# Kernel tuning notes

Measured on AMD Instinct MI355X. Metric: run time of the kernel, lower is better.

Reference implementation:

```python
import jax, jax.numpy as jnp
from jax import lax
import numpy as np

EPS = 1e-5  # BatchNorm eps (inference mode; dropouts are identity in eval)


def _proj(img, w, g, b, m, v, stride):
    """All-heads Conv2d(3x3, no bias) + BatchNorm (inference) fused across heads.
    img: [B, Cin, H, W]; w: [heads, Cout, Cin, 3, 3]; g/b/m/v: [heads, Cout].
    Returns [B, heads, Cout, N'] (channels-first token layout)."""
    heads, Cout, Cin = w.shape[0], w.shape[1], w.shape[2]
    y = lax.conv_general_dilated(
        img, w.reshape(heads * Cout, Cin, 3, 3),
        window_strides=(stride, stride), padding=[(1, 1), (1, 1)],
        dimension_numbers=('NCHW', 'OIHW', 'NCHW'))
    B = y.shape[0]
    N = y.shape[2] * y.shape[3]
    y = y.reshape(B, heads, Cout, N)
    scale = g / jnp.sqrt(v + EPS)               # [heads, Cout]
    shift = b - m * scale
    return y * scale[None, :, :, None] + shift[None, :, :, None]


def reference(x, y, w_conv, bn_gamma, bn_beta, bn_mean, bn_var, w_out1, w_out2, h, w):
    B, N, C = x.shape
    xi = x.reshape(B, h, w, C).transpose(0, 3, 1, 2)  # b (h w) c -> b c h w
    yi = y.reshape(B, h, w, C).transpose(0, 3, 1, 2)
    scale_attn = C ** -0.5

    def P(i, img, stride):
        return _proj(img, w_conv[i], bn_gamma[i], bn_beta[i], bn_mean[i], bn_var[i], stride)

    # torch: query1(x), query2(y), key1(y), key2(x), value1(y), value2(x)
    Q1 = P(0, xi, 2)  # [B,h,C,Nq]
    Q2 = P(1, yi, 2)
    K1 = P(2, yi, 2)
    K2 = P(3, xi, 2)
    V1 = P(4, yi, 1)  # [B,h,C,Nv]
    V2 = P(5, xi, 1)

    # channel-attention: scores are [B, heads, C, C], softmax over last axis
    s1 = jnp.einsum('bhcn,bhdn->bhcd', Q2, K1) * scale_attn
    s2 = jnp.einsum('bhcn,bhdn->bhcd', Q1, K2) * scale_attn
    p1 = jax.nn.softmax(s1, axis=-1)
    p2 = jax.nn.softmax(s2, axis=-1)

    # context [B,heads,C,Nv] -> mean over heads -> [B,Nv,C]
    c1 = jnp.einsum('bhcd,bhdn->bhcn', p1, V1).mean(axis=1).transpose(0, 2, 1)
    c2 = jnp.einsum('bhcd,bhdn->bhcn', p2, V2).mean(axis=1).transpose(0, 2, 1)

    o1 = c1 @ w_out1.T  # Linear(dim_in, dim_out, bias=False)
    o2 = c2 @ w_out2.T
    return o1, o2


def setup_inputs() -> dict:
    B, C, HEADS, H, W = 8, 256, 4, 64, 64
    key = jax.random.key(0)
    ks = jax.random.split(key, 9)
    conv_std = 1.0 / np.sqrt(C * 9)
    lin_std = 1.0 / np.sqrt(C)
    return {
        'x': jax.random.normal(ks[0], (B, H * W, C), jnp.float32),
        'y': jax.random.normal(ks[1], (B, H * W, C), jnp.float32),
        'w_conv': jax.random.normal(ks[2], (6, HEADS, C, C, 3, 3), jnp.float32) * conv_std,
        'bn_gamma': jax.random.uniform(ks[3], (6, HEADS, C), jnp.float32, 0.5, 1.5),
        'bn_beta': jax.random.normal(ks[4], (6, HEADS, C), jnp.float32) * 0.1,
        'bn_mean': jax.random.normal(ks[5], (6, HEADS, C), jnp.float32) * 0.1,
        'bn_var': jax.random.uniform(ks[6], (6, HEADS, C), jnp.float32, 0.5, 1.5),
        'w_out1': jax.random.normal(ks[7], (C, C), jnp.float32) * lin_std,
        'w_out2': jax.random.normal(ks[8], (C, C), jnp.float32) * lin_std,
        'h': H,
        'w': W,
    }
```

## Files before the change

kernel.cpp:

```cpp
#include <hip/hip_runtime.h>
#include <stdint.h>

typedef __bf16 bf16_t;
typedef __bf16 bf16x8 __attribute__((ext_vector_type(8)));
typedef float f32x4 __attribute__((ext_vector_type(4)));

#define EPSBN 1e-5f

#define OFF_XP   ((size_t)0)
#define SZ_IMG   ((size_t)8*4356*256*2)
#define OFF_YP   (OFF_XP + SZ_IMG)
#define OFF_WQS  (OFF_YP + SZ_IMG)
#define SZ_WQS   ((size_t)4*1024*2304*2)
#define OFF_WVT  (OFF_WQS + SZ_WQS)
#define SZ_WVT   ((size_t)2*2304*1024*2)
#define OFF_W1B  (OFF_WVT + SZ_WVT)
#define SZ_WO    ((size_t)65536*2)
#define OFF_W2B  (OFF_W1B + SZ_WO)
#define OFF_SHQ  (OFF_W2B + SZ_WO)
#define SZ_SHQ   ((size_t)4096*4)
#define OFF_SHV  (OFF_SHQ + SZ_SHQ)
#define SZ_SHV   ((size_t)2048*4)
#define OFF_QK   (OFF_SHV + SZ_SHV)
#define SZ_QK    ((size_t)4*8*1024*1024*2)
#define OFF_S    (OFF_QK + SZ_QK)
#define SZ_S     ((size_t)2*8*4*65536*4)
#define OFF_PT   (OFF_S + SZ_S)
#define SZ_PT    ((size_t)2*8*4*65536*2)
#define OFF_A1   (OFF_PT + SZ_PT)
#define SZ_A1    ((size_t)2*8*256*1024*2)
#define OFF_WEFF (OFF_A1 + SZ_A1)
#define SZ_WEFF  ((size_t)2*8*256*2304*2)
#define OFF_BIAS (OFF_WEFF + SZ_WEFF)
#define SZ_BIAS  ((size_t)2*8*256*4)
#define WS_NEED  (OFF_BIAS + SZ_BIAS)

__device__ __forceinline__ void gload16(const bf16_t* g, bf16_t* l) {
  __builtin_amdgcn_global_load_lds(
      (const __attribute__((address_space(1))) void*)g,
      (__attribute__((address_space(3))) void*)l,
      16, 0, 0);
}

__device__ __forceinline__ int lb_off0() { return ((threadIdx.x >> 6)    ) * 512; }
__device__ __forceinline__ int lb_off1() { return ((threadIdx.x >> 6) + 4) * 512; }

#define SBAR0 __builtin_amdgcn_sched_barrier(0)

template<int BSRC>
__device__ __forceinline__ void gemm_core(
    const bf16_t* __restrict__ A, int ldA,
    const bf16_t* __restrict__ B, int ldB,
    int m0, int n0, int KT, f32x4 acc[4][4])
{
  __shared__ bf16_t lA[2][4096];
  __shared__ bf16_t lB[2][4096];
  const int tid  = threadIdx.x;
  const int lane = tid & 63;
  const int wv   = tid >> 6;
  const int wr   = wv >> 1, wc = wv & 1;
  const int r4   = lane >> 2;
  const int k8   = (lane & 3) * 8;

  const bf16_t* gA0 = A + (size_t)(m0 + (wv    )*16 + r4) * ldA + k8;
  const bf16_t* gA1 = A + (size_t)(m0 + (wv + 4)*16 + r4) * ldA + k8;
  const int la0 = (wv    ) * 512;
  const int la1 = (wv + 4) * 512;
  const bf16_t* gB0 = B + (size_t)(n0 + (wv    )*16 + r4) * ldB + k8;
  const bf16_t* gB1 = B + (size_t)(n0 + (wv + 4)*16 + r4) * ldB + k8;
  (void)BSRC;

#pragma unroll
  for (int i = 0; i < 4; ++i)
#pragma unroll
    for (int j = 0; j < 4; ++j)
      acc[i][j] = f32x4{0.f, 0.f, 0.f, 0.f};

  const int lr = lane & 15;
  const int lk = (lane >> 4) * 8;
  int aidx[4], bidx[4];
#pragma unroll
  for (int f = 0; f < 4; ++f) {
    aidx[f] = (wr*64 + f*16 + lr)*32 + lk;
    bidx[f] = (wc*64 + f*16 + lr)*32 + lk;
  }

  auto stage = [&](int bufp, int kt) {
    const int kb = kt * 32;
    gload16(gA0 + kb, &lA[bufp][la0]);
    gload16(gA1 + kb, &lA[bufp][la1]);
    gload16(gB0 + kb, &lB[bufp][lb_off0()]);
    gload16(gB1 + kb, &lB[bufp][lb_off1()]);
  };

  stage(0, 0);
  __syncthreads();
  int buf = 0;
  for (int kt = 0; kt < KT; ++kt) {
    if (kt + 1 < KT) stage(buf ^ 1, kt + 1);
    bf16x8 av[4], bvv[4];
#pragma unroll
    for (int f = 0; f < 4; ++f) av[f]  = *(const bf16x8*)&lA[buf][aidx[f]];
#pragma unroll
    for (int f = 0; f < 4; ++f) bvv[f] = *(const bf16x8*)&lB[buf][bidx[f]];
#pragma unroll
    for (int i = 0; i < 4; ++i)
#pragma unroll
      for (int j = 0; j < 4; ++j)
        acc[i][j] = __builtin_amdgcn_mfma_f32_16x16x32_bf16(av[i], bvv[j], acc[i][j], 0, 0, 0);
    __syncthreads();
    buf ^= 1;
  }
}

template<int STRIDE>
__device__ __forceinline__ void conv256_core(
    const bf16_t* __restrict__ A, const bf16_t* __restrict__ img,
    int m0, int n0, f32x4 acc[8][4])
{
  __shared__ bf16_t lds[4][2][8192];
  const int tid  = threadIdx.x;
  const int lane = tid & 63;
  const int w    = tid >> 6;
  const int wm   = w >> 2;
  const int wn   = w & 3;

#pragma unroll
  for (int f = 0; f < 8; ++f)
#pragma unroll
    for (int j = 0; j < 4; ++j)
      acc[f][j] = f32x4{0.f, 0.f, 0.f, 0.f};

  const int srow = tid >> 2;
  const int ksX  = (tid & 3) ^ ((tid >> 3) & 3);
  const bf16_t* gA0 = A + (size_t)(m0 + srow) * 2304 + ksX*8;
  const bf16_t* gA1 = gA0 + (size_t)128 * 2304;
  const int tk0 = n0 + srow, tk1 = tk0 + 128;
  int px0, px1;
  if (STRIDE == 1) { px0 = (tk0>>6)*66 + (tk0&63);       px1 = (tk1>>6)*66 + (tk1&63); }
  else             { px0 = ((tk0>>5)*2)*66 + (tk0&31)*2; px1 = ((tk1>>5)*2)*66 + (tk1&31)*2; }
  const bf16_t* gB0 = img + (size_t)px0*256 + ksX*8;
  const bf16_t* gB1 = img + (size_t)px1*256 + ksX*8;

  auto stageHalf = [&](int half) {
    const int s = half & 3;
    bf16_t* dA = &lds[s][0][0] + tid*8;
    gload16(gA0 + half*32, dA);
    gload16(gA1 + half*32, dA + 4096);
    const int T = half >> 1, kh = half & 1;
    const int tap = T >> 2;
    const int ky  = (tap >= 6) ? 2 : ((tap >= 3) ? 1 : 0);
    const int kx  = tap - ky*3;
    const int ps  = (ky*66 + kx)*256 + (T & 3)*64 + kh*32;
    bf16_t* dB = &lds[s][1][0] + tid*8;
    gload16(gB0 + ps, dB);
    gload16(gB1 + ps, dB + 4096);
  };

  const int lr    = lane & 15;
  const int slotS = (lane >> 4) ^ ((lane & 6) >> 1);
  int offA[8], offB[4];
#pragma unroll
  for (int f = 0; f < 8; ++f)  offA[f] = (wm*128 + f*16 + lr)*32 + slotS*8;
#pragma unroll
  for (int n = 0; n < 4; ++n)  offB[n] = (wn*64  + n*16 + lr)*32 + slotS*8;

#define LOADREGS(HALF, AV, BV) do {                                        \
    const int s_ = (HALF) & 3;                                             \
    const bf16_t* pA_ = &lds[s_][0][0];                                    \
    const bf16_t* pB_ = &lds[s_][1][0];                                    \
    _Pragma("unroll") for (int f_ = 0; f_ < 8; ++f_)                       \
      AV[f_] = *(const bf16x8*)(pA_ + offA[f_]);                           \
    _Pragma("unroll") for (int n_ = 0; n_ < 4; ++n_)                       \
      BV[n_] = *(const bf16x8*)(pB_ + offB[n_]);                           \
  } while (0)

#define MFMA32(AV, BV) do {                                                \
    __builtin_amdgcn_s_setprio(1);                                         \
    _Pragma("unroll") for (int f_ = 0; f_ < 8; ++f_)                       \
      _Pragma("unroll") for (int n_ = 0; n_ < 4; ++n_)                     \
        acc[f_][n_] = __builtin_amdgcn_mfma_f32_16x16x32_bf16(             \
            AV[f_], BV[n_], acc[f_][n_], 0, 0, 0);                         \
    __builtin_amdgcn_s_setprio(0);                                         \
  } while (0)

  stageHalf(0); stageHalf(1); stageHalf(2);
  SBAR0;
  asm volatile("s_waitcnt vmcnt(4)" ::: "memory");
  SBAR0;
  __builtin_amdgcn_s_barrier();
  SBAR0;

  bf16x8 avP[8], bvP[4], avN[8], bvN[4];
  LOADREGS(0, avP, bvP);

  for (int h = 0; h < 72; h += 2) {
    if (h + 3 < 72) stageHalf(h + 3);
    LOADREGS(h + 1, avN, bvN);
    SBAR0;
    if (h < 69) { asm volatile("s_waitcnt vmcnt(4)" ::: "memory"); }
    else        { asm volatile("s_waitcnt vmcnt(0)" ::: "memory"); }
    SBAR0;
    asm volatile("s_waitcnt lgkmcnt(12)" ::: "memory");
    SBAR0;
    MFMA32(avP, bvP);
    __builtin_amdgcn_s_barrier();
    SBAR0;

    const int h1 = h + 1;
    if (h1 + 3 < 72) stageHalf(h1 + 3);
    if (h1 < 71) {
      LOADREGS(h1 + 1, avP, bvP);
      SBAR0;
      if (h1 < 69) { asm volatile("s_waitcnt vmcnt(4)" ::: "memory"); }
      else         { asm volatile("s_waitcnt vmcnt(0)" ::: "memory"); }
      SBAR0;
      asm volatile("s_waitcnt lgkmcnt(12)" ::: "memory");
      SBAR0;
    } else {
      SBAR0;
      asm volatile("s_waitcnt lgkmcnt(0)" ::: "memory");
      SBAR0;
    }
    MFMA32(avN, bvN);
    __builtin_amdgcn_s_barrier();
    SBAR0;
  }
#undef LOADREGS
#undef MFMA32
}

__global__ __launch_bounds__(512, 2) void k_conv_qk2(const bf16_t* __restrict__ wqs,
    const bf16_t* __restrict__ xp, const bf16_t* __restrict__ yp,
    bf16_t* __restrict__ qk, const float* __restrict__ shq)
{
  const int bx = blockIdx.x, b = blockIdx.y, ci = blockIdx.z;
  const int mt = bx >> 2, nt = bx & 3;
  const int m0 = mt*256, n0 = nt*256;
  const bf16_t* A = wqs + (size_t)ci * 1024 * 2304;
  const bf16_t* img = (((ci == 0) | (ci == 3)) ? xp : yp) + (size_t)b*4356*256;
  f32x4 acc[8][4];
  conv256_core<2>(A, img, m0, n0, acc);

  bf16_t* out = qk + (size_t)(ci*8 + b) * 1024 * 1024;
  const float* sh = shq + ci*1024;
  const int lane = threadIdx.x & 63, w = threadIdx.x >> 6;
  const int wm = w >> 2, wn = w & 3;
#pragma unroll
  for (int f = 0; f < 8; ++f) {
    const int row0 = m0 + wm*128 + f*16 + ((lane >> 4) << 2);
    const f32x4 s4 = *(const f32x4*)&sh[row0];
#pragma unroll
    for (int nf = 0; nf < 4; ++nf) {
      const int col = n0 + wn*64 + nf*16 + (lane & 15);
#pragma unroll
      for (int r = 0; r < 4; ++r)
        out[(size_t)(row0 + r)*1024 + col] = (bf16_t)(acc[f][nf][r] + s4[r]);
    }
  }
}

__global__ __launch_bounds__(512, 2) void k_conv_out2(const bf16_t* __restrict__ weff,
    const bf16_t* __restrict__ xp, const bf16_t* __restrict__ yp,
    const float* __restrict__ bias, float* __restrict__ dout)
{
  const int nt = blockIdx.x, b = blockIdx.y, br = blockIdx.z;
  const int n0 = nt*256;
  const bf16_t* A = weff + (size_t)(br*8 + b)*589824;
  const bf16_t* img = ((br == 0) ? yp : xp) + (size_t)b*4356*256;
  f32x4 acc[8][4];
  conv256_core<1>(A, img, 0, n0, acc);

  float* outp = dout + (size_t)br*8388608 + (size_t)b*1048576;
  const float* bp = bias + (size_t)(br*8 + b)*256;
  const int lane = threadIdx.x & 63, w = threadIdx.x >> 6;
  const int wm = w >> 2, wn = w & 3;
#pragma unroll
  for (int f = 0; f < 8; ++f) {
    const int e0 = wm*128 + f*16 + ((lane >> 4) << 2);
    const f32x4 bv4 = *(const f32x4*)&bp[e0];
#pragma unroll
    for (int nf = 0; nf < 4; ++nf) {
      const int tok = n0 + wn*64 + nf*16 + (lane & 15);
      f32x4 v = acc[f][nf] + bv4;
      *(f32x4*)&outp[(size_t)tok*256 + e0] = v;
    }
  }
}

__global__ __launch_bounds__(256) void k_pack(const float* __restrict__ x, const float* __restrict__ y,
                                              bf16_t* __restrict__ xp, bf16_t* __restrict__ yp)
{
  const int p  = blockIdx.x;
  const int b  = blockIdx.y;
  const int im = blockIdx.z;
  const int c  = threadIdx.x;
  const int i = p / 66, j = p - i*66;
  const float* src = im ? y : x;
  bf16_t* dst = im ? yp : xp;
  float v = 0.f;
  if (i >= 1 && i <= 64 && j >= 1 && j <= 64)
    v = src[((size_t)b*4096 + (size_t)(i-1)*64 + (j-1))*256 + c];
  dst[((size_t)b*4356 + p)*256 + c] = (bf16_t)v;
}

__global__ __launch_bounds__(256) void k_prep_wq(const float* __restrict__ wcv,
    const float* __restrict__ g, const float* __restrict__ be,
    const float* __restrict__ mu, const float* __restrict__ va,
    bf16_t* __restrict__ wqs, float* __restrict__ shq)
{
  const int blk = blockIdx.x;
  __shared__ float lw[2304];
  const float* src = wcv + (size_t)blk * 2304;
  for (int t = threadIdx.x; t < 2304; t += 256) lw[t] = src[t];
  const float sc = g[blk] * rsqrtf(va[blk] + EPSBN);
  if (threadIdx.x == 0) shq[blk] = be[blk] - mu[blk]*sc;
  __syncthreads();
  bf16_t* dst = wqs + (size_t)blk * 2304;
  for (int t = threadIdx.x; t < 2304; t += 256) {
    const int tap = t >> 8, c = t & 255;
    dst[t] = (bf16_t)(lw[c*9 + tap] * sc);
  }
}

__global__ __launch_bounds__(256) void k_prep_wv(const float* __restrict__ wcv,
    const float* __restrict__ g, const float* __restrict__ va,
    bf16_t* __restrict__ wvT)
{
  const int cch = blockIdx.x;
  const int h = blockIdx.y >> 2, dc = blockIdx.y & 3;
  const int br = blockIdx.z;
  __shared__ float lw[64][72];
  __shared__ float lsc[64];
  const int ci = 4 + br;
  const int c0 = cch*8, d0 = dc*64;
  for (int e = threadIdx.x; e < 64*72; e += 256) {
    const int dd = e / 72, q = e - dd*72;
    lw[dd][q] = wcv[(size_t)(ci*1024 + h*256 + d0 + dd)*2304 + c0*9 + q];
  }
  if (threadIdx.x < 64) {
    const int bnIdx = ci*1024 + h*256 + d0 + threadIdx.x;
    lsc[threadIdx.x] = g[bnIdx] * rsqrtf(va[bnIdx] + EPSBN);
  }
  __syncthreads();
  for (int e = threadIdx.x; e < 72*64; e += 256) {
    const int kq = e >> 6, dd = e & 63;
    const int cc = kq / 9, tap = kq - cc*9;
    const int kp = tap*256 + c0 + cc;
    wvT[(size_t)br*2359296 + (size_t)kp*1024 + h*256 + d0 + dd] =
        (bf16_t)(lw[dd][cc*9 + tap] * lsc[dd]);
  }
}

__global__ __launch_bounds__(256) void k_small(const float* __restrict__ w1, const float* __restrict__ w2,
    const float* __restrict__ g, const float* __restrict__ be,
    const float* __restrict__ mu, const float* __restrict__ va,
    bf16_t* __restrict__ w1b, bf16_t* __restrict__ w2b, float* __restrict__ shv)
{
  const int idx = blockIdx.x*256 + threadIdx.x;
  if (idx < 65536) {
    w1b[idx] = (bf16_t)w1[idx];
  } else if (idx < 131072) {
    w2b[idx - 65536] = (bf16_t)w2[idx - 65536];
  } else if (idx < 133120) {
    const int t = idx - 131072;
    const int bnIdx = 4096 + t;
    const float sc = g[bnIdx] * rsqrtf(va[bnIdx] + EPSBN);
    shv[t] = be[bnIdx] - mu[bnIdx]*sc;
  }
}

__global__ __launch_bounds__(256) void k_gemm_s(const bf16_t* __restrict__ qk, float* __restrict__ sb)
{
  const int bx = blockIdx.x, by = blockIdx.y, br = blockIdx.z;
  const int mt = bx >> 1, nt = bx & 1;
  const int b = by >> 2, h = by & 3;
  const int ai = (br == 0) ? 1 : 0;
  const int bi = (br == 0) ? 2 : 3;
  const bf16_t* A  = qk + ((size_t)(ai*8 + b)*1024 + h*256) * 1024;
  const bf16_t* Bp = qk + ((size_t)(bi*8 + b)*1024 + h*256) * 1024;
  f32x4 acc[4][4];
  gemm_core<0>(A, 1024, Bp, 1024, mt*128, nt*128, 32, acc);

  float* out = sb + ((size_t)(br*8 + b)*4 + h) * 65536;
  const int lane = threadIdx.x & 63, wv = threadIdx.x >> 6;
  const int wr = wv >> 1, wc = wv & 1;
#pragma unroll
  for (int i = 0; i < 4; ++i) {
    const int row0 = mt*128 + wr*64 + i*16 + ((lane >> 4) << 2);
#pragma unroll
    for (int j = 0; j < 4; ++j) {
      const int col = nt*128 + wc*64 + j*16 + (lane & 15);
#pragma unroll
      for (int r = 0; r < 4; ++r)
        out[(size_t)(row0 + r)*256 + col] = acc[i][j][r];
    }
  }
}

__global__ __launch_bounds__(256) void k_softmax(const float* __restrict__ sb, bf16_t* __restrict__ pt)
{
  const int cc = blockIdx.x;
  const int bh = blockIdx.y;
  const int br = blockIdx.z;
  const size_t base = ((size_t)br*32 + bh) * 65536;
  __shared__ bf16_t lp[32][256];
  const int tid = threadIdx.x, lane = tid & 63, wv = tid >> 6;
  for (int r = 0; r < 8; ++r) {
    const int row = wv*8 + r;
    const float* srow = sb + base + (size_t)(cc*32 + row)*256;
    f32x4 v = ((const f32x4*)srow)[lane];
    v *= 0.0625f;
    float m = fmaxf(fmaxf(v[0], v[1]), fmaxf(v[2], v[3]));
#pragma unroll
    for (int o = 32; o; o >>= 1) m = fmaxf(m, __shfl_xor(m, o));
    const float e0 = __expf(v[0]-m), e1 = __expf(v[1]-m), e2 = __expf(v[2]-m), e3 = __expf(v[3]-m);
    float s = e0+e1+e2+e3;
#pragma unroll
    for (int o = 32; o; o >>= 1) s += __shfl_xor(s, o);
    const float inv = 0.25f / s;
    lp[row][lane*4+0] = (bf16_t)(e0*inv);
    lp[row][lane*4+1] = (bf16_t)(e1*inv);
    lp[row][lane*4+2] = (bf16_t)(e2*inv);
    lp[row][lane*4+3] = (bf16_t)(e3*inv);
  }
  __syncthreads();
  bf16_t* dst = pt + base;
  for (int it = 0; it < 32; ++it) {
    const int idx = it*256 + tid;
    const int d = idx >> 5, c = idx & 31;
    dst[(size_t)d*256 + cc*32 + c] = lp[c][d];
  }
}

__global__ __launch_bounds__(256) void k_gemm_a(const bf16_t* __restrict__ w1b, const bf16_t* __restrict__ w2b,
    const bf16_t* __restrict__ pt, bf16_t* __restrict__ a1)
{
  const int bx = blockIdx.x, by = blockIdx.y, br = blockIdx.z;
  const int mt = bx >> 1, nt = bx & 1;
  const int b = by >> 2, h = by & 3;
  const bf16_t* A  = br ? w2b : w1b;
  const bf16_t* Bp = pt + ((size_t)(br*8 + b)*4 + h) * 65536;
  f32x4 acc[4][4];
  gemm_core<0>(A, 256, Bp, 256, mt*128, nt*128, 8, acc);

  bf16_t* out = a1 + (size_t)(br*8 + b)*262144 + h*256;
  const int lane = threadIdx.x & 63, wv = threadIdx.x >> 6;
  const int wr = wv >> 1, wc = wv & 1;
#pragma unroll
  for (int i = 0; i < 4; ++i) {
    const int row0 = mt*128 + wr*64 + i*16 + ((lane >> 4) << 2);
#pragma unroll
    for (int j = 0; j < 4; ++j) {
      const int col = nt*128 + wc*64 + j*16 + (lane & 15);
#pragma unroll
      for (int r = 0; r < 4; ++r)
        out[(size_t)(row0 + r)*1024 + col] = (bf16_t)acc[i][j][r];
    }
  }
}

__global__ __launch_bounds__(256) void k_bias(const bf16_t* __restrict__ a1,
    const float* __restrict__ shv, float* __restrict__ bias)
{
  const int wv = threadIdx.x >> 6, lane = threadIdx.x & 63;
  const int e = blockIdx.x*4 + wv;
  const int b = blockIdx.y, br = blockIdx.z;
  const bf16_t* row = a1 + ((size_t)(br*8 + b)*256 + e)*1024;
  const float* sv = shv + br*1024;
  float acc = 0.f;
#pragma unroll
  for (int t = 0; t < 16; ++t) {
    const int idx = t*64 + lane;
    acc += (float)row[idx] * sv[idx];
  }
#pragma unroll
  for (int o = 32; o; o >>= 1) acc += __shfl_xor(acc, o);
  if (lane == 0) bias[(size_t)(br*8 + b)*256 + e] = acc;
}

__global__ __launch_bounds__(256) void k_gemm_weff(const bf16_t* __restrict__ a1,
    const bf16_t* __restrict__ wvT, bf16_t* __restrict__ weff)
{
  const int bx = blockIdx.x, b = blockIdx.y, br = blockIdx.z;
  const int mt = bx / 18, nt = bx - mt*18;
  const bf16_t* A  = a1 + (size_t)(br*8 + b)*262144;
  const bf16_t* Bp = wvT + (size_t)br*2359296;
  f32x4 acc[4][4];
  gemm_core<0>(A, 1024, Bp, 1024, mt*128, nt*128, 32, acc);

  bf16_t* out = weff + (size_t)(br*8 + b)*589824;
  const int lane = threadIdx.x & 63, wv = threadIdx.x >> 6;
  const int wr = wv >> 1, wc = wv & 1;
#pragma unroll
  for (int i = 0; i < 4; ++i) {
    const int row0 = mt*128 + wr*64 + i*16 + ((lane >> 4) << 2);
#pragma unroll
    for (int j = 0; j < 4; ++j) {
      const int col = nt*128 + wc*64 + j*16 + (lane & 15);
#pragma unroll
      for (int r = 0; r < 4; ++r)
        out[(size_t)(row0 + r)*2304 + col] = (bf16_t)acc[i][j][r];
    }
  }
}

extern "C" void kernel_launch(void* const* d_in, const int* in_sizes, int n_in,
                              void* d_out, int out_size, void* d_ws, size_t ws_size,
                              hipStream_t stream)
{
  (void)in_sizes; (void)n_in; (void)out_size;
  const float* x   = (const float*)d_in[0];
  const float* y   = (const float*)d_in[1];
  const float* wcv = (const float*)d_in[2];
  const float* bg  = (const float*)d_in[3];
  const float* bb  = (const float*)d_in[4];
  const float* bm  = (const float*)d_in[5];
  const float* bvv = (const float*)d_in[6];
  const float* w1  = (const float*)d_in[7];
  const float* w2  = (const float*)d_in[8];
  float* out = (float*)d_out;
  char* ws = (char*)d_ws;
  if (ws_size < WS_NEED) return;

  bf16_t* xp   = (bf16_t*)(ws + OFF_XP);
  bf16_t* yp   = (bf16_t*)(ws + OFF_YP);
  bf16_t* wqs  = (bf16_t*)(ws + OFF_WQS);
  bf16_t* wvT  = (bf16_t*)(ws + OFF_WVT);
  bf16_t* w1b  = (bf16_t*)(ws + OFF_W1B);
  bf16_t* w2b  = (bf16_t*)(ws + OFF_W2B);
  float*  shq  = (float*)(ws + OFF_SHQ);
  float*  shv  = (float*)(ws + OFF_SHV);
  bf16_t* qk   = (bf16_t*)(ws + OFF_QK);
  float*  sb   = (float*)(ws + OFF_S);
  bf16_t* pt   = (bf16_t*)(ws + OFF_PT);
  bf16_t* a1   = (bf16_t*)(ws + OFF_A1);
  bf16_t* weff = (bf16_t*)(ws + OFF_WEFF);
  float*  bias = (float*)(ws + OFF_BIAS);

  k_pack     <<<dim3(4356, 8, 2), 256, 0, stream>>>(x, y, xp, yp);
  k_prep_wq  <<<dim3(4096), 256, 0, stream>>>(wcv, bg, bb, bm, bvv, wqs, shq);
  k_prep_wv  <<<dim3(32, 16, 2), 256, 0, stream>>>(wcv, bg, bvv, wvT);
  k_small    <<<dim3(520), 256, 0, stream>>>(w1, w2, bg, bb, bm, bvv, w1b, w2b, shv);
  k_conv_qk2 <<<dim3(16, 8, 4), 512, 0, stream>>>(wqs, xp, yp, qk, shq);
  k_gemm_s   <<<dim3(4, 32, 2), 256, 0, stream>>>(qk, sb);
  k_softmax  <<<dim3(8, 32, 2), 256, 0, stream>>>(sb, pt);
  k_gemm_a   <<<dim3(4, 32, 2), 256, 0, stream>>>(w1b, w2b, pt, a1);
  k_bias     <<<dim3(64, 8, 2), 256, 0, stream>>>(a1, shv, bias);
  k_gemm_weff<<<dim3(36, 8, 2), 256, 0, stream>>>(a1, wvT, weff);
  k_conv_out2<<<dim3(16, 8, 2), 512, 0, stream>>>(weff, xp, yp, bias, out);
}
```

Before: 368.4 us.

## Shrink conv tiles to 256x128 with six-stage LDS pipeline and batch-fastest grid

The shared implicit-GEMM conv core now computes 256x128 output tiles instead of 256x256. Each wave handles 64x64 instead of 128x64, and the B operand is staged as a single 128-token slab. The LDS ring deepens from 4 to 6 stages, so global loads are issued five steps ahead, and the register double-buffer is replaced by a per-step load then MFMA with barriers. Both conv launches move to a 1D grid with batch as the fastest index, doubling block counts to better fill the CUs and group blocks that share weights. In exchange, each block reuses its operands less and pays more barriers per step.

```diff
diff --git a/kernel.cpp b/kernel.cpp
--- a/kernel.cpp
+++ b/kernel.cpp
@@ -114,37 +114,37 @@
 }
 
 template<int STRIDE>
-__device__ __forceinline__ void conv256_core(
+__device__ __forceinline__ void conv128_core(
     const bf16_t* __restrict__ A, const bf16_t* __restrict__ img,
-    int m0, int n0, f32x4 acc[8][4])
-{
-  __shared__ bf16_t lds[4][2][8192];
+    int m0, int n0, f32x4 acc[4][4])
+{
+  __shared__ bf16_t ldsA[6][8192];
+  __shared__ bf16_t ldsB[6][4096];
   const int tid  = threadIdx.x;
   const int lane = tid & 63;
   const int w    = tid >> 6;
-  const int wm   = w >> 2;
-  const int wn   = w & 3;
-
-#pragma unroll
-  for (int f = 0; f < 8; ++f)
-#pragma unroll
-    for (int j = 0; j < 4; ++j)
-      acc[f][j] = f32x4{0.f, 0.f, 0.f, 0.f};
+  const int wm   = w >> 1;
+  const int wn   = w & 1;
+
+#pragma unroll
+  for (int f = 0; f < 4; ++f)
+#pragma unroll
+    for (int c = 0; c < 4; ++c)
+      acc[f][c] = f32x4{0.f, 0.f, 0.f, 0.f};
 
   const int srow = tid >> 2;
   const int ksX  = (tid & 3) ^ ((tid >> 3) & 3);
   const bf16_t* gA0 = A + (size_t)(m0 + srow) * 2304 + ksX*8;
   const bf16_t* gA1 = gA0 + (size_t)128 * 2304;
-  const int tk0 = n0 + srow, tk1 = tk0 + 128;
-  int px0, px1;
-  if (STRIDE == 1) { px0 = (tk0>>6)*66 + (tk0&63);       px1 = (tk1>>6)*66 + (tk1&63); }
-  else             { px0 = ((tk0>>5)*2)*66 + (tk0&31)*2; px1 = ((tk1>>5)*2)*66 + (tk1&31)*2; }
+  const int tk0 = n0 + srow;
+  int px0;
+  if (STRIDE == 1) px0 = (tk0>>6)*66 + (tk0&63);
+  else             px0 = ((tk0>>5)*2)*66 + (tk0&31)*2;
   const bf16_t* gB0 = img + (size_t)px0*256 + ksX*8;
-  const bf16_t* gB1 = img + (size_t)px1*256 + ksX*8;
 
   auto stageHalf = [&](int half) {
-    const int s = half & 3;
-    bf16_t* dA = &lds[s][0][0] + tid*8;
+    const int sl = half % 6;
+    bf16_t* dA = &ldsA[sl][0] + tid*8;
     gload16(gA0 + half*32, dA);
     gload16(gA1 + half*32, dA + 4096);
     const int T = half >> 1, kh = half & 1;
@@ -152,137 +152,120 @@
     const int ky  = (tap >= 6) ? 2 : ((tap >= 3) ? 1 : 0);
     const int kx  = tap - ky*3;
     const int ps  = (ky*66 + kx)*256 + (T & 3)*64 + kh*32;
-    bf16_t* dB = &lds[s][1][0] + tid*8;
-    gload16(gB0 + ps, dB);
-    gload16(gB1 + ps, dB + 4096);
+    gload16(gB0 + ps, &ldsB[sl][0] + tid*8);
   };
 
   const int lr    = lane & 15;
   const int slotS = (lane >> 4) ^ ((lane & 6) >> 1);
-  int offA[8], offB[4];
-#pragma unroll
-  for (int f = 0; f < 8; ++f)  offA[f] = (wm*128 + f*16 + lr)*32 + slotS*8;
-#pragma unroll
-  for (int n = 0; n < 4; ++n)  offB[n] = (wn*64  + n*16 + lr)*32 + slotS*8;
-
-#define LOADREGS(HALF, AV, BV) do {                                        \
-    const int s_ = (HALF) & 3;                                             \
-    const bf16_t* pA_ = &lds[s_][0][0];                                    \
-    const bf16_t* pB_ = &lds[s_][1][0];                                    \
-    _Pragma("unroll") for (int f_ = 0; f_ < 8; ++f_)                       \
-      AV[f_] = *(const bf16x8*)(pA_ + offA[f_]);                           \
-    _Pragma("unroll") for (int n_ = 0; n_ < 4; ++n_)                       \
-      BV[n_] = *(const bf16x8*)(pB_ + offB[n_]);                           \
-  } while (0)
-
-#define MFMA32(AV, BV) do {                                                \
-    __builtin_amdgcn_s_setprio(1);                                         \
-    _Pragma("unroll") for (int f_ = 0; f_ < 8; ++f_)                       \
-      _Pragma("unroll") for (int n_ = 0; n_ < 4; ++n_)                     \
-        acc[f_][n_] = __builtin_amdgcn_mfma_f32_16x16x32_bf16(             \
-            AV[f_], BV[n_], acc[f_][n_], 0, 0, 0);                         \
-    __builtin_amdgcn_s_setprio(0);                                         \
-  } while (0)
-
-  stageHalf(0); stageHalf(1); stageHalf(2);
+  int offA[4], offB[4];
+#pragma unroll
+  for (int f = 0; f < 4; ++f) offA[f] = (wm*64 + f*16 + lr)*32 + slotS*8;
+#pragma unroll
+  for (int c = 0; c < 4; ++c) offB[c] = (wn*64 + c*16 + lr)*32 + slotS*8;
+
+  stageHalf(0); stageHalf(1); stageHalf(2); stageHalf(3); stageHalf(4);
   SBAR0;
-  asm volatile("s_waitcnt vmcnt(4)" ::: "memory");
+  asm volatile("s_waitcnt vmcnt(12)" ::: "memory");
   SBAR0;
   __builtin_amdgcn_s_barrier();
   SBAR0;
 
-  bf16x8 avP[8], bvP[4], avN[8], bvN[4];
-  LOADREGS(0, avP, bvP);
-
-  for (int h = 0; h < 72; h += 2) {
-    if (h + 3 < 72) stageHalf(h + 3);
-    LOADREGS(h + 1, avN, bvN);
+  for (int p = 0; p < 72; ++p) {
+    const int sl = p % 6;
+    const bf16_t* pA = &ldsA[sl][0];
+    const bf16_t* pB = &ldsB[sl][0];
+    bf16x8 av[4], bv[4];
+#pragma unroll
+    for (int f = 0; f < 4; ++f) av[f] = *(const bf16x8*)(pA + offA[f]);
+#pragma unroll
+    for (int c = 0; c < 4; ++c) bv[c] = *(const bf16x8*)(pB + offB[c]);
+    if (p + 5 < 72) stageHalf(p + 5);
     SBAR0;
-    if (h < 69) { asm volatile("s_waitcnt vmcnt(4)" ::: "memory"); }
-    else        { asm volatile("s_waitcnt vmcnt(0)" ::: "memory"); }
+    if      (p < 67)  { asm volatile("s_waitcnt vmcnt(12)" ::: "memory"); }
+    else if (p == 67) { asm volatile("s_waitcnt vmcnt(9)"  ::: "memory"); }
+    else if (p == 68) { asm volatile("s_waitcnt vmcnt(6)"  ::: "memory"); }
+    else if (p == 69) { asm volatile("s_waitcnt vmcnt(3)"  ::: "memory"); }
+    else if (p == 70) { asm volatile("s_waitcnt vmcnt(0)"  ::: "memory"); }
     SBAR0;
-    asm volatile("s_waitcnt lgkmcnt(12)" ::: "memory");
+    asm volatile("s_waitcnt lgkmcnt(4)" ::: "memory");
     SBAR0;
-    MFMA32(avP, bvP);
+    __builtin_amdgcn_s_barrier();
+    asm volatile("s_waitcnt lgkmcnt(0)" ::: "memory");
+    SBAR0;
+    __builtin_amdgcn_s_setprio(1);
+#pragma unroll
+    for (int f = 0; f < 4; ++f)
+#pragma unroll
+      for (int c = 0; c < 4; ++c)
+        acc[f][c] = __builtin_amdgcn_mfma_f32_16x16x32_bf16(av[f], bv[c], acc[f][c], 0, 0, 0);
+    __builtin_amdgcn_s_setprio(0);
     __builtin_amdgcn_s_barrier();
     SBAR0;
-
-    const int h1 = h + 1;
-    if (h1 + 3 < 72) stageHalf(h1 + 3);
-    if (h1 < 71) {
-      LOADREGS(h1 + 1, avP, bvP);
-      SBAR0;
-      if (h1 < 69) { asm volatile("s_waitcnt vmcnt(4)" ::: "memory"); }
-      else         { asm volatile("s_waitcnt vmcnt(0)" ::: "memory"); }
-      SBAR0;
-      asm volatile("s_waitcnt lgkmcnt(12)" ::: "memory");
-      SBAR0;
-    } else {
-      SBAR0;
-      asm volatile("s_waitcnt lgkmcnt(0)" ::: "memory");
-      SBAR0;
-    }
-    MFMA32(avN, bvN);
-    __builtin_amdgcn_s_barrier();
-    SBAR0;
-  }
-#undef LOADREGS
-#undef MFMA32
-}
-
-__global__ __launch_bounds__(512, 2) void k_conv_qk2(const bf16_t* __restrict__ wqs,
+  }
+}
+
+__global__ __launch_bounds__(512, 2) void k_conv_qk3(const bf16_t* __restrict__ wqs,
     const bf16_t* __restrict__ xp, const bf16_t* __restrict__ yp,
     bf16_t* __restrict__ qk, const float* __restrict__ shq)
 {
-  const int bx = blockIdx.x, b = blockIdx.y, ci = blockIdx.z;
-  const int mt = bx >> 2, nt = bx & 3;
-  const int m0 = mt*256, n0 = nt*256;
+  const int n  = blockIdx.x;
+  const int b  = n & 7;
+  const int r1 = n >> 3;
+  const int ci = r1 & 3;
+  const int t  = r1 >> 2;
+  const int mt = t >> 3;
+  const int nt = t & 7;
+  const int m0 = mt*256, n0 = nt*128;
   const bf16_t* A = wqs + (size_t)ci * 1024 * 2304;
   const bf16_t* img = (((ci == 0) | (ci == 3)) ? xp : yp) + (size_t)b*4356*256;
-  f32x4 acc[8][4];
-  conv256_core<2>(A, img, m0, n0, acc);
+  f32x4 acc[4][4];
+  conv128_core<2>(A, img, m0, n0, acc);
 
   bf16_t* out = qk + (size_t)(ci*8 + b) * 1024 * 1024;
   const float* sh = shq + ci*1024;
   const int lane = threadIdx.x & 63, w = threadIdx.x >> 6;
-  const int wm = w >> 2, wn = w & 3;
-#pragma unroll
-  for (int f = 0; f < 8; ++f) {
-    const int row0 = m0 + wm*128 + f*16 + ((lane >> 4) << 2);
+  const int wm = w >> 1, wn = w & 1;
+#pragma unroll
+  for (int f = 0; f < 4; ++f) {
+    const int row0 = m0 + wm*64 + f*16 + ((lane >> 4) << 2);
     const f32x4 s4 = *(const f32x4*)&sh[row0];
 #pragma unroll
-    for (int nf = 0; nf < 4; ++nf) {
-      const int col = n0 + wn*64 + nf*16 + (lane & 15);
+    for (int c = 0; c < 4; ++c) {
+      const int col = n0 + wn*64 + c*16 + (lane & 15);
 #pragma unroll
       for (int r = 0; r < 4; ++r)
-        out[(size_t)(row0 + r)*1024 + col] = (bf16_t)(acc[f][nf][r] + s4[r]);
+        out[(size_t)(row0 + r)*1024 + col] = (bf16_t)(acc[f][c][r] + s4[r]);
     }
   }
 }
 
-__global__ __launch_bounds__(512, 2) void k_conv_out2(const bf16_t* __restrict__ weff,
+__global__ __launch_bounds__(512, 2) void k_conv_out3(const bf16_t* __restrict__ weff,
     const bf16_t* __restrict__ xp, const bf16_t* __restrict__ yp,
     const float* __restrict__ bias, float* __restrict__ dout)
 {
-  const int nt = blockIdx.x, b = blockIdx.y, br = blockIdx.z;
-  const int n0 = nt*256;
+  const int n  = blockIdx.x;
+  const int b  = n & 7;
+  const int r1 = n >> 3;
+  const int br = r1 & 1;
+  const int nt = r1 >> 1;
+  const int n0 = nt*128;
   const bf16_t* A = weff + (size_t)(br*8 + b)*589824;
   const bf16_t* img = ((br == 0) ? yp : xp) + (size_t)b*4356*256;
-  f32x4 acc[8][4];
-  conv256_core<1>(A, img, 0, n0, acc);
+  f32x4 acc[4][4];
+  conv128_core<1>(A, img, 0, n0, acc);
 
   float* outp = dout + (size_t)br*8388608 + (size_t)b*1048576;
   const float* bp = bias + (size_t)(br*8 + b)*256;
   const int lane = threadIdx.x & 63, w = threadIdx.x >> 6;
-  const int wm = w >> 2, wn = w & 3;
-#pragma unroll
-  for (int f = 0; f < 8; ++f) {
-    const int e0 = wm*128 + f*16 + ((lane >> 4) << 2);
+  const int wm = w >> 1, wn = w & 1;
+#pragma unroll
+  for (int f = 0; f < 4; ++f) {
+    const int e0 = wm*64 + f*16 + ((lane >> 4) << 2);
     const f32x4 bv4 = *(const f32x4*)&bp[e0];
 #pragma unroll
-    for (int nf = 0; nf < 4; ++nf) {
-      const int tok = n0 + wn*64 + nf*16 + (lane & 15);
-      f32x4 v = acc[f][nf] + bv4;
+    for (int c = 0; c < 4; ++c) {
+      const int tok = n0 + wn*64 + c*16 + (lane & 15);
+      f32x4 v = acc[f][c] + bv4;
       *(f32x4*)&outp[(size_t)tok*256 + e0] = v;
     }
   }
@@ -542,11 +525,11 @@
   k_prep_wq  <<<dim3(4096), 256, 0, stream>>>(wcv, bg, bb, bm, bvv, wqs, shq);
   k_prep_wv  <<<dim3(32, 16, 2), 256, 0, stream>>>(wcv, bg, bvv, wvT);
   k_small    <<<dim3(520), 256, 0, stream>>>(w1, w2, bg, bb, bm, bvv, w1b, w2b, shv);
-  k_conv_qk2 <<<dim3(16, 8, 4), 512, 0, stream>>>(wqs, xp, yp, qk, shq);
+  k_conv_qk3 <<<dim3(1024), 512, 0, stream>>>(wqs, xp, yp, qk, shq);
   k_gemm_s   <<<dim3(4, 32, 2), 256, 0, stream>>>(qk, sb);
   k_softmax  <<<dim3(8, 32, 2), 256, 0, stream>>>(sb, pt);
   k_gemm_a   <<<dim3(4, 32, 2), 256, 0, stream>>>(w1b, w2b, pt, a1);
   k_bias     <<<dim3(64, 8, 2), 256, 0, stream>>>(a1, shv, bias);
   k_gemm_weff<<<dim3(36, 8, 2), 256, 0, stream>>>(a1, wvT, weff);
-  k_conv_out2<<<dim3(16, 8, 2), 512, 0, stream>>>(weff, xp, yp, bias, out);
-}
+  k_conv_out3<<<dim3(512), 512, 0, stream>>>(weff, xp, yp, bias, out);
+}
```

After: 444.8 us. 1.21x slower.
